# Performance work log

Hardware: AMD Instinct MI355X
Metric: run time of the kernel (lower is better)

The kernel has to match this reference:

```python
import jax, jax.numpy as jnp
import numpy as np
from jax import lax

V, E, H = 32000, 512, 512
B, S = 64, 512

def setup_inputs() -> dict:
    key = jax.random.key(0)
    k1, k2, k3, k4, k5 = jax.random.split(key, 5)
    bound = 1.0 / np.sqrt(H)  # torch nn.RNN init: U(-1/sqrt(H), 1/sqrt(H))
    return {
        "input_tensor": jax.random.randint(k1, (B, S), 0, V, dtype=jnp.int64),
        "emb": jax.random.normal(k2, (V, E), dtype=jnp.float32),  # nn.Embedding ~ N(0,1)
        "W_ih": jax.random.uniform(k3, (H, E), jnp.float32, -bound, bound),
        "W_hh": jax.random.uniform(k4, (H, H), jnp.float32, -bound, bound),
        "b_ih": jax.random.uniform(k5, (H,), jnp.float32, -bound, bound),
        "b_hh": jax.random.uniform(jax.random.fold_in(key, 7), (H,), jnp.float32, -bound, bound),
    }

def reference(input_tensor, emb, W_ih, W_hh, b_ih, b_hh):
    # Embedding lookup: (B, S, E)
    x = emb[input_tensor]
    # Precompute input projection for all timesteps (batched GEMM): (B, S, H)
    x_proj = jnp.einsum("bse,he->bsh", x, W_ih) + b_ih + b_hh
    h0 = jnp.zeros((B, H), dtype=x.dtype)

    def step(h, xp_t):  # xp_t: (B, H)
        h_new = jnp.tanh(xp_t + h @ W_hh.T)
        return h_new, h_new

    hT, outs = lax.scan(step, h0, jnp.swapaxes(x_proj, 0, 1))  # outs: (S, B, H)
    outputs = jnp.swapaxes(outs, 0, 1)  # (B, S, H), batch_first
    hidden = hT[None]  # (1, B, H) matching torch (num_layers, B, H)
    return outputs, hidden
```

## Files before the change

### kernel.cpp

```cpp
#include <hip/hip_runtime.h>
#include <cstdint>

#define BB 64
#define SS 512
#define HH 512
#define EE 512
#define BSH (BB*SS*HH)

typedef _Float16 f16x8 __attribute__((ext_vector_type(8)));
typedef float    f32x4 __attribute__((ext_vector_type(4)));
typedef int      iv4   __attribute__((ext_vector_type(4)));
typedef unsigned long long u64;

__device__ __forceinline__ f16x8 pack8(float4 u, float4 v) {
    f16x8 h;
    h[0] = (_Float16)u.x; h[1] = (_Float16)u.y;
    h[2] = (_Float16)u.z; h[3] = (_Float16)u.w;
    h[4] = (_Float16)v.x; h[5] = (_Float16)v.y;
    h[6] = (_Float16)v.z; h[7] = (_Float16)v.w;
    return h;
}

#define SW (127.0f * 22.627416997969522f)

__device__ __forceinline__ int quanw(float x) {
    return (int)rintf(fminf(fmaxf(x * SW, -127.0f), 127.0f));
}
__device__ __forceinline__ int packw4(float4 f) {
    int q0 = quanw(f.x), q1 = quanw(f.y), q2 = quanw(f.z), q3 = quanw(f.w);
    return (q0 & 255) | ((q1 & 255) << 8) | ((q2 & 255) << 16) | (q3 << 24);
}

__device__ __forceinline__ void gload16(const void* g, void* l) {
    __builtin_amdgcn_global_load_lds(
        (const __attribute__((address_space(1))) void*)g,
        (__attribute__((address_space(3))) void*)l, 16, 0, 0);
}

__device__ __forceinline__ void wait_tile(const unsigned int* c, unsigned int tgt) {
    while (__hip_atomic_load(c, __ATOMIC_RELAXED, __HIP_MEMORY_SCOPE_AGENT) < tgt) {
        __builtin_amdgcn_s_sleep(2);
    }
    __builtin_amdgcn_fence(__ATOMIC_ACQUIRE, "agent");
}

__global__ __launch_bounds__(256) void prep(
    const int* __restrict__ idx, const float* __restrict__ emb,
    const float* __restrict__ Wih, _Float16* __restrict__ a16,
    _Float16* __restrict__ b16) {
    const int bid = blockIdx.x, tid = threadIdx.x;
    if (bid < 8192) {
        int e = bid * 2048 + tid * 8;
        int m = e >> 9, c = e & 511;
        int gi = idx[m];
        const float* s = emb + (size_t)gi * EE + c;
        float4 u = *(const float4*)s, v = *(const float4*)(s + 4);
        *(f16x8*)(a16 + e) = pack8(u, v);
    } else {
        int e = (bid - 8192) * 2048 + tid * 8;
        float4 u = *(const float4*)(Wih + e), v = *(const float4*)(Wih + e + 4);
        *(f16x8*)(b16 + e) = pack8(u, v);
    }
}

__global__ __launch_bounds__(512, 1) void fused12(
    const _Float16* __restrict__ a16, const _Float16* __restrict__ b16,
    const float* __restrict__ bih, const float* __restrict__ bhh,
    const float* __restrict__ Whh, float* __restrict__ out,
    unsigned int* __restrict__ cnt) {
    __shared__ __align__(16) unsigned char smem[32768];

    const int tid  = threadIdx.x;
    const int bid  = blockIdx.x;
    const int wv   = tid >> 6;
    const int lane = tid & 63;
    const int n    = lane & 15;
    const int quad = lane >> 4;

    if (bid >= 64) {
        _Float16* Al = (_Float16*)smem;
        _Float16* Bl = (_Float16*)(smem + 16384);
        const int p  = bid - 64;
        const int st = p >> 8;
        const int r  = p & 255;
        const int bb = r >> 2;
        const int nt = r & 3;
        const int m0 = bb * 512 + st * 128;
        const int n0 = nt * 128;

        const int srow = wv * 16 + (lane >> 3);
        const int scol = (lane & 7) * 8;
        const _Float16* agl = a16 + (size_t)(m0 + srow) * EE + scol;
        const _Float16* bgl = b16 + (size_t)(n0 + srow) * EE + scol;
        _Float16* al = Al + wv * 1024;
        _Float16* bl = Bl + wv * 1024;

        const int mw = wv >> 2;
        const int nw = wv & 3;

        f32x4 acc[4][2];
#pragma unroll
        for (int mb = 0; mb < 4; ++mb)
#pragma unroll
            for (int nb = 0; nb < 2; ++nb) acc[mb][nb] = (f32x4){0.f, 0.f, 0.f, 0.f};

        for (int kc = 0; kc < 8; ++kc) {
            gload16(agl + kc * 64,               al);
            gload16(agl + (size_t)8 * EE + kc * 64, al + 512);
            gload16(bgl + kc * 64,               bl);
            gload16(bgl + (size_t)8 * EE + kc * 64, bl + 512);
            __syncthreads();

#pragma unroll
            for (int kk = 0; kk < 2; ++kk) {
                f16x8 bfr[2];
#pragma unroll
                for (int nb = 0; nb < 2; ++nb)
                    bfr[nb] = *(const f16x8*)&Bl[(nw * 32 + nb * 16 + n) * 64 + kk * 32 + quad * 8];
#pragma unroll
                for (int mb = 0; mb < 4; ++mb) {
                    f16x8 afr = *(const f16x8*)&Al[(mw * 64 + mb * 16 + n) * 64 + kk * 32 + quad * 8];
#pragma unroll
                    for (int nb = 0; nb < 2; ++nb)
                        acc[mb][nb] = __builtin_amdgcn_mfma_f32_16x16x32_f16(
                            afr, bfr[nb], acc[mb][nb], 0, 0, 0);
                }
            }
            __syncthreads();
        }

        int   cc[2];
        float bv[2];
#pragma unroll
        for (int nb = 0; nb < 2; ++nb) {
            cc[nb] = n0 + nw * 32 + nb * 16 + n;
            bv[nb] = bih[cc[nb]] + bhh[cc[nb]];
        }
#pragma unroll
        for (int mb = 0; mb < 4; ++mb) {
            int rowg = m0 + mw * 64 + mb * 16 + quad * 4;
#pragma unroll
            for (int nb = 0; nb < 2; ++nb) {
#pragma unroll
                for (int i = 0; i < 4; ++i)
                    out[(size_t)(rowg + i) * HH + cc[nb]] = acc[mb][nb][i] + bv[nb];
            }
        }
        __asm__ volatile("s_waitcnt vmcnt(0)" ::: "memory");
        __syncthreads();
        if (tid == 0) {
            __builtin_amdgcn_fence(__ATOMIC_RELEASE, "agent");
            __hip_atomic_fetch_add(cnt + st, 1u, __ATOMIC_RELAXED,
                                   __HIP_MEMORY_SCOPE_AGENT);
        }
        return;
    }

    unsigned char* h0p = smem;
    unsigned char* h1p = smem + 512;
    const int b = bid;

    iv4 areg[4][8];
#pragma unroll
    for (int mb = 0; mb < 4; ++mb) {
        const float* wr = Whh + (size_t)(wv * 64 + mb * 16 + n) * HH + quad * 16;
#pragma unroll
        for (int j = 0; j < 8; ++j) {
            int kb = (j < 7) ? ((wv + 1 + j) & 7) : wv;
            const float4* ptr = (const float4*)(wr + kb * 64);
            iv4 v;
            v[0] = packw4(ptr[0]);
            v[1] = packw4(ptr[1]);
            v[2] = packw4(ptr[2]);
            v[3] = packw4(ptr[3]);
            areg[mb][j] = v;
        }
    }
    if (tid < 64) ((u64*)h0p)[tid] = 0ull;
    __syncthreads();

    const int  ilo = n & 1;
    const int  ihi = (n >> 1) & 1;
    const bool sb0 = ((n >> 2) & 1) != 0;
    const bool sb1 = ((n >> 3) & 1) != 0;
    const int  row = wv * 64 + ((n >> 2) & 3) * 16 + quad * 4 + (n & 3);
    float* obase = out + (size_t)b * (SS * HH) + row;

    int koff[7];
#pragma unroll
    for (int j = 0; j < 7; ++j) koff[j] = ((wv + 1 + j) & 7) * 64 + quad * 16;
    const int oown = wv * 64 + quad * 16;

    const float inv2 = (2.0f * 1.4426950408889634f) / (SW * 127.0f);
    const float K2   = 2.0f * 1.4426950408889634f;

    iv4 acc0 = (iv4){0,0,0,0}, acc1 = (iv4){0,0,0,0};
    iv4 acc2 = (iv4){0,0,0,0}, acc3 = (iv4){0,0,0,0};

    wait_tile(cnt, 256u);
    float xp2_c = obase[0] * K2;
    float xp2_n = obase[HH] * K2;
    float hl = 0.f;

#define RNN_STEP(T, HBR, HNX)                                                  \
    {                                                                          \
        if ((((T) + 2) & 127) == 0 && ((T) + 2) < SS)                          \
            wait_tile(cnt + (((T) + 2) >> 7), 256u);                           \
        float xp_f = obase[(size_t)((T) + 2) * HH];                            \
        _Pragma("unroll")                                                      \
        for (int j = 0; j < 7; ++j) {                                          \
            iv4 bfr = *(const iv4*)((HBR) + koff[j]);                          \
            acc0 = __builtin_amdgcn_mfma_i32_16x16x64_i8(areg[0][j], bfr, acc0, 0, 0, 0); \
            acc1 = __builtin_amdgcn_mfma_i32_16x16x64_i8(areg[1][j], bfr, acc1, 0, 0, 0); \
            acc2 = __builtin_amdgcn_mfma_i32_16x16x64_i8(areg[2][j], bfr, acc2, 0, 0, 0); \
            acc3 = __builtin_amdgcn_mfma_i32_16x16x64_i8(areg[3][j], bfr, acc3, 0, 0, 0); \
        }                                                                      \
        iv4 sa = sb0 ? acc1 : acc0;                                            \
        iv4 sc = sb0 ? acc3 : acc2;                                            \
        iv4 s  = sb1 ? sc : sa;                                                \
        int zA = ilo ? s[1] : s[0];                                            \
        int zB = ilo ? s[3] : s[2];                                            \
        int z  = ihi ? zB : zA;                                                \
        float u  = fmaf((float)z, inv2, xp2_c);                                \
        float ex;                                                              \
        __asm__("v_exp_f32 %0, %1" : "=v"(ex) : "v"(u));                       \
        float rr = __builtin_amdgcn_rcpf(ex + 1.0f);                           \
        int   q  = (int)rintf(fmaf(rr, -254.0f, 127.0f));                      \
        *(char*)((HNX) + row) = (char)q;                                       \
        iv4 bown = *(const iv4*)((HNX) + oown);                                \
        acc0 = __builtin_amdgcn_mfma_i32_16x16x64_i8(areg[0][7], bown, (iv4){0,0,0,0}, 0, 0, 0); \
        acc1 = __builtin_amdgcn_mfma_i32_16x16x64_i8(areg[1][7], bown, (iv4){0,0,0,0}, 0, 0, 0); \
        acc2 = __builtin_amdgcn_mfma_i32_16x16x64_i8(areg[2][7], bown, (iv4){0,0,0,0}, 0, 0, 0); \
        acc3 = __builtin_amdgcn_mfma_i32_16x16x64_i8(areg[3][7], bown, (iv4){0,0,0,0}, 0, 0, 0); \
        float h = fmaf(rr, -2.0f, 1.0f);                                       \
        obase[(size_t)(T) * HH] = h;                                           \
        hl = h;                                                                \
        __builtin_amdgcn_sched_barrier(0);                                     \
        __asm__ volatile("s_waitcnt lgkmcnt(0)\n\ts_barrier" ::: "memory");    \
        xp2_c = xp2_n; xp2_n = xp_f * K2;                                      \
    }

    for (int t = 0; t < SS; t += 2) {
        RNN_STEP(t,     h0p, h1p);
        RNN_STEP(t + 1, h1p, h0p);
    }
#undef RNN_STEP

    out[BSH + (size_t)b * HH + row] = hl;
}

__global__ __launch_bounds__(256, 3) void phase1(
    const int* __restrict__ idx, const float* __restrict__ emb,
    const float* __restrict__ Wih, const float* __restrict__ bih,
    const float* __restrict__ bhh, float* __restrict__ out) {
    __shared__ __align__(16) _Float16 Al[128 * 72];
    __shared__ __align__(16) _Float16 Bl[128 * 72];

    const int tid  = threadIdx.x;
    const int m0   = (blockIdx.x >> 2) * 128;
    const int n0   = (blockIdx.x & 3) * 128;
    const int wv   = tid >> 6;
    const int lane = tid & 63;
    const int n    = lane & 15;
    const int quad = lane >> 4;
    const int mw   = wv >> 1;
    const int nw   = wv & 1;

    const int sr = tid >> 1;
    const int kh = (tid & 1) * 32;
    const int rowidx = idx[m0 + sr];
    const float* ap = emb + (size_t)rowidx * EE + kh;
    const float* bp = Wih + (size_t)(n0 + sr) * EE + kh;

    f32x4 acc[4][4];
#pragma unroll
    for (int a = 0; a < 4; ++a)
#pragma unroll
        for (int c = 0; c < 4; ++c) acc[a][c] = (f32x4){0.f, 0.f, 0.f, 0.f};

    for (int kc = 0; kc < 8; ++kc) {
#pragma unroll
        for (int q = 0; q < 4; ++q) {
            float4 u = *(const float4*)(ap + kc * 64 + q * 8);
            float4 v = *(const float4*)(ap + kc * 64 + q * 8 + 4);
            *(f16x8*)&Al[sr * 72 + kh + q * 8] = pack8(u, v);
        }
#pragma unroll
        for (int q = 0; q < 4; ++q) {
            float4 u = *(const float4*)(bp + kc * 64 + q * 8);
            float4 v = *(const float4*)(bp + kc * 64 + q * 8 + 4);
            *(f16x8*)&Bl[sr * 72 + kh + q * 8] = pack8(u, v);
        }
        __syncthreads();

#pragma unroll
        for (int kk = 0; kk < 2; ++kk) {
            f16x8 bfr[4];
#pragma unroll
            for (int nb = 0; nb < 4; ++nb)
                bfr[nb] = *(const f16x8*)&Bl[(nw * 64 + nb * 16 + n) * 72 + kk * 32 + quad * 8];
#pragma unroll
            for (int mb = 0; mb < 4; ++mb) {
                f16x8 afr = *(const f16x8*)&Al[(mw * 64 + mb * 16 + n) * 72 + kk * 32 + quad * 8];
#pragma unroll
                for (int nb = 0; nb < 4; ++nb)
                    acc[mb][nb] = __builtin_amdgcn_mfma_f32_16x16x32_f16(
                        afr, bfr[nb], acc[mb][nb], 0, 0, 0);
            }
        }
        __syncthreads();
    }

    int   cc[4];
    float bv[4];
#pragma unroll
    for (int nb = 0; nb < 4; ++nb) {
        cc[nb] = n0 + nw * 64 + nb * 16 + n;
        bv[nb] = bih[cc[nb]] + bhh[cc[nb]];
    }
#pragma unroll
    for (int mb = 0; mb < 4; ++mb) {
        int rowg = m0 + mw * 64 + mb * 16 + quad * 4;
#pragma unroll
        for (int nb = 0; nb < 4; ++nb) {
#pragma unroll
            for (int i = 0; i < 4; ++i)
                out[(size_t)(rowg + i) * HH + cc[nb]] = acc[mb][nb][i] + bv[nb];
        }
    }
}

__global__ __launch_bounds__(512, 1) void phase2(
    const float* __restrict__ Whh, float* __restrict__ out) {
    __shared__ __align__(16) unsigned char himg[2][512];

    const int tid  = threadIdx.x;
    const int b    = blockIdx.x;
    const int wv   = tid >> 6;
    const int lane = tid & 63;
    const int n    = lane & 15;
    const int quad = lane >> 4;

    iv4 areg[4][8];
#pragma unroll
    for (int mb = 0; mb < 4; ++mb) {
        const float* wr = Whh + (size_t)(wv * 64 + mb * 16 + n) * HH + quad * 16;
#pragma unroll
        for (int j = 0; j < 8; ++j) {
            int kb = (j < 7) ? ((wv + 1 + j) & 7) : wv;
            const float4* p = (const float4*)(wr + kb * 64);
            iv4 v;
            v[0] = packw4(p[0]);
            v[1] = packw4(p[1]);
            v[2] = packw4(p[2]);
            v[3] = packw4(p[3]);
            areg[mb][j] = v;
        }
    }
    if (tid < 64) ((u64*)himg[0])[tid] = 0ull;
    __syncthreads();

    const int  ilo = n & 1;
    const int  ihi = (n >> 1) & 1;
    const bool sb0 = ((n >> 2) & 1) != 0;
    const bool sb1 = ((n >> 3) & 1) != 0;
    const int  row = wv * 64 + ((n >> 2) & 3) * 16 + quad * 4 + (n & 3);
    float* obase = out + (size_t)b * (SS * HH) + row;

    int koff[7];
#pragma unroll
    for (int j = 0; j < 7; ++j) koff[j] = ((wv + 1 + j) & 7) * 64 + quad * 16;
    const int oown = wv * 64 + quad * 16;

    const float inv2 = (2.0f * 1.4426950408889634f) / (SW * 127.0f);
    const float K2   = 2.0f * 1.4426950408889634f;

    iv4 acc0 = (iv4){0,0,0,0}, acc1 = (iv4){0,0,0,0};
    iv4 acc2 = (iv4){0,0,0,0}, acc3 = (iv4){0,0,0,0};

    float xp2_c = obase[0] * K2;
    float xp2_n = obase[HH] * K2;
    float hl = 0.f;
    unsigned char* h0p = himg[0];
    unsigned char* h1p = himg[1];

#define RNN_STEP(T, HBR, HNX)                                                  \
    {                                                                          \
        float xp_f = obase[(size_t)((T) + 2) * HH];                            \
        _Pragma("unroll")                                                      \
        for (int j = 0; j < 7; ++j) {                                          \
            iv4 bfr = *(const iv4*)((HBR) + koff[j]);                          \
            acc0 = __builtin_amdgcn_mfma_i32_16x16x64_i8(areg[0][j], bfr, acc0, 0, 0, 0); \
            acc1 = __builtin_amdgcn_mfma_i32_16x16x64_i8(areg[1][j], bfr, acc1, 0, 0, 0); \
            acc2 = __builtin_amdgcn_mfma_i32_16x16x64_i8(areg[2][j], bfr, acc2, 0, 0, 0); \
            acc3 = __builtin_amdgcn_mfma_i32_16x16x64_i8(areg[3][j], bfr, acc3, 0, 0, 0); \
        }                                                                      \
        iv4 sa = sb0 ? acc1 : acc0;                                            \
        iv4 sc = sb0 ? acc3 : acc2;                                            \
        iv4 s  = sb1 ? sc : sa;                                                \
        int zA = ilo ? s[1] : s[0];                                            \
        int zB = ilo ? s[3] : s[2];                                            \
        int z  = ihi ? zB : zA;                                                \
        float u  = fmaf((float)z, inv2, xp2_c);                                \
        float ex;                                                              \
        __asm__("v_exp_f32 %0, %1" : "=v"(ex) : "v"(u));                       \
        float rr = __builtin_amdgcn_rcpf(ex + 1.0f);                           \
        int   q  = (int)rintf(fmaf(rr, -254.0f, 127.0f));                      \
        *(char*)((HNX) + row) = (char)q;                                       \
        iv4 bown = *(const iv4*)((HNX) + oown);                                \
        acc0 = __builtin_amdgcn_mfma_i32_16x16x64_i8(areg[0][7], bown, (iv4){0,0,0,0}, 0, 0, 0); \
        acc1 = __builtin_amdgcn_mfma_i32_16x16x64_i8(areg[1][7], bown, (iv4){0,0,0,0}, 0, 0, 0); \
        acc2 = __builtin_amdgcn_mfma_i32_16x16x64_i8(areg[2][7], bown, (iv4){0,0,0,0}, 0, 0, 0); \
        acc3 = __builtin_amdgcn_mfma_i32_16x16x64_i8(areg[3][7], bown, (iv4){0,0,0,0}, 0, 0, 0); \
        float h = fmaf(rr, -2.0f, 1.0f);                                       \
        obase[(size_t)(T) * HH] = h;                                           \
        hl = h;                                                                \
        __builtin_amdgcn_sched_barrier(0);                                     \
        __asm__ volatile("s_waitcnt lgkmcnt(0)\n\ts_barrier" ::: "memory");    \
        xp2_c = xp2_n; xp2_n = xp_f * K2;                                      \
    }

    for (int t = 0; t < SS; t += 2) {
        RNN_STEP(t,     h0p, h1p);
        RNN_STEP(t + 1, h1p, h0p);
    }
#undef RNN_STEP

    out[BSH + (size_t)b * HH + row] = hl;
}

extern "C" void kernel_launch(void* const* d_in, const int* in_sizes, int n_in,
                              void* d_out, int out_size, void* d_ws, size_t ws_size,
                              hipStream_t stream) {
    const int*   idx = (const int*)d_in[0];
    const float* emb = (const float*)d_in[1];
    const float* Wih = (const float*)d_in[2];
    const float* Whh = (const float*)d_in[3];
    const float* bih = (const float*)d_in[4];
    const float* bhh = (const float*)d_in[5];
    float* out = (float*)d_out;

    const size_t needA = (size_t)BB * SS * EE * sizeof(_Float16);
    const size_t needB = (size_t)HH * EE * sizeof(_Float16);
    const size_t CNTOFF = needA + needB;
    const size_t needT = CNTOFF + 4 * sizeof(unsigned int);

    if (d_ws && ws_size >= needT) {
        _Float16* a16 = (_Float16*)d_ws;
        _Float16* b16 = (_Float16*)((char*)d_ws + needA);
        unsigned int* cnt = (unsigned int*)((char*)d_ws + CNTOFF);
        hipMemsetAsync(cnt, 0, 4 * sizeof(unsigned int), stream);
        prep<<<dim3(8192 + 128), dim3(256), 0, stream>>>(idx, emb, Wih, a16, b16);
        fused12<<<dim3(64 + 1024), dim3(512), 0, stream>>>(
            a16, b16, bih, bhh, Whh, out, cnt);
    } else {
        phase1<<<dim3(1024), dim3(256), 0, stream>>>(idx, emb, Wih, bih, bhh, out);
        phase2<<<dim3(64), dim3(512), 0, stream>>>(Whh, out);
    }
}
```

Baseline: 553.0 us.

## Fuse embedding gather and fp16 conversion into GEMM; per-batch tile counters

```diff
diff --git a/kernel.cpp b/kernel.cpp
--- a/kernel.cpp
+++ b/kernel.cpp
@@ -31,11 +31,7 @@
     return (q0 & 255) | ((q1 & 255) << 8) | ((q2 & 255) << 16) | (q3 << 24);
 }
 
-__device__ __forceinline__ void gload16(const void* g, void* l) {
-    __builtin_amdgcn_global_load_lds(
-        (const __attribute__((address_space(1))) void*)g,
-        (__attribute__((address_space(3))) void*)l, 16, 0, 0);
-}
+#define SWZ(row, off) ((row) * 64 + ((off) ^ (((row) & 7) << 3)))
 
 __device__ __forceinline__ void wait_tile(const unsigned int* c, unsigned int tgt) {
     while (__hip_atomic_load(c, __ATOMIC_RELAXED, __HIP_MEMORY_SCOPE_AGENT) < tgt) {
@@ -44,27 +40,9 @@
     __builtin_amdgcn_fence(__ATOMIC_ACQUIRE, "agent");
 }
 
-__global__ __launch_bounds__(256) void prep(
+__global__ __launch_bounds__(512, 1) void fused12(
     const int* __restrict__ idx, const float* __restrict__ emb,
-    const float* __restrict__ Wih, _Float16* __restrict__ a16,
-    _Float16* __restrict__ b16) {
-    const int bid = blockIdx.x, tid = threadIdx.x;
-    if (bid < 8192) {
-        int e = bid * 2048 + tid * 8;
-        int m = e >> 9, c = e & 511;
-        int gi = idx[m];
-        const float* s = emb + (size_t)gi * EE + c;
-        float4 u = *(const float4*)s, v = *(const float4*)(s + 4);
-        *(f16x8*)(a16 + e) = pack8(u, v);
-    } else {
-        int e = (bid - 8192) * 2048 + tid * 8;
-        float4 u = *(const float4*)(Wih + e), v = *(const float4*)(Wih + e + 4);
-        *(f16x8*)(b16 + e) = pack8(u, v);
-    }
-}
-
-__global__ __launch_bounds__(512, 1) void fused12(
-    const _Float16* __restrict__ a16, const _Float16* __restrict__ b16,
+    const float* __restrict__ Wih,
     const float* __restrict__ bih, const float* __restrict__ bhh,
     const float* __restrict__ Whh, float* __restrict__ out,
     unsigned int* __restrict__ cnt) {
@@ -82,18 +60,18 @@
         _Float16* Bl = (_Float16*)(smem + 16384);
         const int p  = bid - 64;
         const int st = p >> 8;
-        const int r  = p & 255;
-        const int bb = r >> 2;
-        const int nt = r & 3;
+        const int bb = (p >> 2) & 63;
+        const int nt = p & 3;
         const int m0 = bb * 512 + st * 128;
         const int n0 = nt * 128;
 
-        const int srow = wv * 16 + (lane >> 3);
-        const int scol = (lane & 7) * 8;
-        const _Float16* agl = a16 + (size_t)(m0 + srow) * EE + scol;
-        const _Float16* bgl = b16 + (size_t)(n0 + srow) * EE + scol;
-        _Float16* al = Al + wv * 1024;
-        _Float16* bl = Bl + wv * 1024;
+        const int arow = tid >> 2;
+        const int coff = (tid & 3) * 16;
+        const int rowidx = idx[m0 + arow];
+        const float* ap = emb + (size_t)rowidx * EE + coff;
+        const float* bp = Wih + (size_t)(n0 + arow) * EE + coff;
+        const int woff0 = SWZ(arow, coff);
+        const int woff1 = SWZ(arow, coff + 8);
 
         const int mw = wv >> 2;
         const int nw = wv & 3;
@@ -105,10 +83,16 @@
             for (int nb = 0; nb < 2; ++nb) acc[mb][nb] = (f32x4){0.f, 0.f, 0.f, 0.f};
 
         for (int kc = 0; kc < 8; ++kc) {
-            gload16(agl + kc * 64,               al);
-            gload16(agl + (size_t)8 * EE + kc * 64, al + 512);
-            gload16(bgl + kc * 64,               bl);
-            gload16(bgl + (size_t)8 * EE + kc * 64, bl + 512);
+            {
+                const float4* la = (const float4*)(ap + kc * 64);
+                const float4* lb = (const float4*)(bp + kc * 64);
+                float4 a0 = la[0], a1 = la[1], a2 = la[2], a3 = la[3];
+                float4 b0 = lb[0], b1 = lb[1], b2 = lb[2], b3 = lb[3];
+                *(f16x8*)&Al[woff0] = pack8(a0, a1);
+                *(f16x8*)&Al[woff1] = pack8(a2, a3);
+                *(f16x8*)&Bl[woff0] = pack8(b0, b1);
+                *(f16x8*)&Bl[woff1] = pack8(b2, b3);
+            }
             __syncthreads();
 
 #pragma unroll
@@ -116,10 +100,10 @@
                 f16x8 bfr[2];
 #pragma unroll
                 for (int nb = 0; nb < 2; ++nb)
-                    bfr[nb] = *(const f16x8*)&Bl[(nw * 32 + nb * 16 + n) * 64 + kk * 32 + quad * 8];
+                    bfr[nb] = *(const f16x8*)&Bl[SWZ(nw * 32 + nb * 16 + n, kk * 32 + quad * 8)];
 #pragma unroll
                 for (int mb = 0; mb < 4; ++mb) {
-                    f16x8 afr = *(const f16x8*)&Al[(mw * 64 + mb * 16 + n) * 64 + kk * 32 + quad * 8];
+                    f16x8 afr = *(const f16x8*)&Al[SWZ(mw * 64 + mb * 16 + n, kk * 32 + quad * 8)];
 #pragma unroll
                     for (int nb = 0; nb < 2; ++nb)
                         acc[mb][nb] = __builtin_amdgcn_mfma_f32_16x16x32_f16(
@@ -150,7 +134,7 @@
         __syncthreads();
         if (tid == 0) {
             __builtin_amdgcn_fence(__ATOMIC_RELEASE, "agent");
-            __hip_atomic_fetch_add(cnt + st, 1u, __ATOMIC_RELAXED,
+            __hip_atomic_fetch_add(cnt + st * 64 + bb, 1u, __ATOMIC_RELAXED,
                                    __HIP_MEMORY_SCOPE_AGENT);
         }
         return;
@@ -197,7 +181,7 @@
     iv4 acc0 = (iv4){0,0,0,0}, acc1 = (iv4){0,0,0,0};
     iv4 acc2 = (iv4){0,0,0,0}, acc3 = (iv4){0,0,0,0};
 
-    wait_tile(cnt, 256u);
+    wait_tile(cnt + b, 4u);
     float xp2_c = obase[0] * K2;
     float xp2_n = obase[HH] * K2;
     float hl = 0.f;
@@ -205,7 +189,7 @@
 #define RNN_STEP(T, HBR, HNX)                                                  \
     {                                                                          \
         if ((((T) + 2) & 127) == 0 && ((T) + 2) < SS)                          \
-            wait_tile(cnt + (((T) + 2) >> 7), 256u);                           \
+            wait_tile(cnt + ((((T) + 2) >> 7) * 64 + b), 4u);                  \
         float xp_f = obase[(size_t)((T) + 2) * HH];                            \
         _Pragma("unroll")                                                      \
         for (int j = 0; j < 7; ++j) {                                          \
@@ -440,19 +424,13 @@
     const float* bhh = (const float*)d_in[5];
     float* out = (float*)d_out;
 
-    const size_t needA = (size_t)BB * SS * EE * sizeof(_Float16);
-    const size_t needB = (size_t)HH * EE * sizeof(_Float16);
-    const size_t CNTOFF = needA + needB;
-    const size_t needT = CNTOFF + 4 * sizeof(unsigned int);
-
-    if (d_ws && ws_size >= needT) {
-        _Float16* a16 = (_Float16*)d_ws;
-        _Float16* b16 = (_Float16*)((char*)d_ws + needA);
-        unsigned int* cnt = (unsigned int*)((char*)d_ws + CNTOFF);
-        hipMemsetAsync(cnt, 0, 4 * sizeof(unsigned int), stream);
-        prep<<<dim3(8192 + 128), dim3(256), 0, stream>>>(idx, emb, Wih, a16, b16);
+    const size_t CNTBYTES = 256 * sizeof(unsigned int);
+
+    if (d_ws && ws_size >= CNTBYTES) {
+        unsigned int* cnt = (unsigned int*)d_ws;
+        hipMemsetAsync(cnt, 0, CNTBYTES, stream);
         fused12<<<dim3(64 + 1024), dim3(512), 0, stream>>>(
-            a16, b16, bih, bhh, Whh, out, cnt);
+            idx, emb, Wih, bih, bhh, Whh, out, cnt);
     } else {
         phase1<<<dim3(1024), dim3(256), 0, stream>>>(idx, emb, Wih, bih, bhh, out);
         phase2<<<dim3(64), dim3(512), 0, stream>>>(Whh, out);
```

Result: no change. 548.7 us (-0.8%).
